# Kernel optimization log

Measured on AMD Instinct MI355X. Metric: run time of the kernel, lower is better.

Reference implementation:

```python
import jax, jax.numpy as jnp
import numpy as np

B, CIN, COUT, H, W, K = 32, 256, 256, 56, 56, 3
STRIDE, PAD, DIL = 1, 1, 1
SPARSITY = 0.9  # fraction of weight entries pruned to zero


def setup_inputs() -> dict:
    key = jax.random.key(0)
    kx, kw, km = jax.random.split(key, 3)
    x = jax.random.normal(kx, (B, CIN, H, W), dtype=jnp.float32)
    w = jax.random.normal(kw, (COUT, CIN, K, K), dtype=jnp.float32)
    mask = (jax.random.uniform(km, (COUT, CIN, K, K)) > SPARSITY).astype(jnp.float32)
    w = w * mask
    return {"x": x, "weight": w}


def reference(x, weight):
    # Faithful math of SparseConv2D.forward (sparse path == nn.Conv2d, bias=None):
    # NCHW input, OIHW weight, stride/pad/dilation as configured.
    out = jax.lax.conv_general_dilated(
        x, weight,
        window_strides=(STRIDE, STRIDE),
        padding=[(PAD, PAD), (PAD, PAD)],
        rhs_dilation=(DIL, DIL),
        dimension_numbers=("NCHW", "OIHW", "NCHW"),
    )
    return out  # [B, COUT, H_out, W_out]
```

## Files before the change

kernel.cpp:

```cpp
#include <hip/hip_runtime.h>
#include <hip/hip_bf16.h>


typedef __attribute__((ext_vector_type(8))) short short8;
typedef __attribute__((ext_vector_type(4))) float f32x4;
typedef __attribute__((ext_vector_type(4))) int i32x4;

constexpr int BB = 32, CIN = 256, COUT = 256, H = 56, W = 56, HW = H * W;
constexpr int HP = 58, WP = 58;
constexpr int XSTR = 40, WSTR = 40;

constexpr size_t XP_ELEMS = (size_t)BB * HP * WP * CIN;
constexpr size_t WB_ELEMS = (size_t)COUT * 9 * CIN;
constexpr size_t WS_NEEDED = (XP_ELEMS + WB_ELEMS) * 2;

__device__ __forceinline__ ushort f2bf(float f) {
    unsigned x = __float_as_uint(f);
    unsigned r = (x + 0x7FFFu + ((x >> 16) & 1u)) >> 16;
    return (ushort)r;
}


__global__ __launch_bounds__(256)
void prep_xp(const float* __restrict__ x, ushort* __restrict__ xp) {
    const int bi = blockIdx.x;
    const int b = bi / HP, i = bi % HP;
    ushort* dst = xp + (size_t)bi * WP * CIN;
    const int t = threadIdx.x;
    if (i == 0 || i == HP - 1) {
        for (int c = 0; c < WP; ++c) dst[c * CIN + t] = 0;
    } else {
        const float* src = x + ((size_t)b * CIN + t) * HW + (size_t)(i - 1) * W;
        dst[0 * CIN + t] = 0;
        dst[(WP - 1) * CIN + t] = 0;
        for (int c = 1; c <= W; ++c)
            dst[c * CIN + t] = f2bf(src[c - 1]);
    }
}

__global__ __launch_bounds__(256)
void prep_wb(const float* __restrict__ w, ushort* __restrict__ wb) {
    const int d = blockIdx.x * 256 + threadIdx.x;
    const int cin = d & 255;
    const int rest = d >> 8;
    const int tap = rest % 9;
    const int cout = rest / 9;
    wb[d] = f2bf(w[((size_t)cout * CIN + cin) * 9 + tap]);
}


__global__ __launch_bounds__(256)
void conv_mfma(const ushort* __restrict__ xp, const ushort* __restrict__ wb,
               float* __restrict__ out) {
    int bx = blockIdx.x;
    bx = (bx & 7) * 224 + (bx >> 3);

    const int mt = bx & 1;
    const int nt = bx >> 1;
    const int b  = nt / 28;
    const int h0 = (nt % 28) * 2;

    const int tid  = threadIdx.x;
    const int wv   = tid >> 6;
    const int lane = tid & 63;
    const int ml   = lane & 15;
    const int g    = lane >> 4;

    __shared__ ushort xs[4 * WP * XSTR];
    __shared__ ushort wt[128 * WSTR];

    const int aoff0 = (wv * 32 + ml) * WSTR + 8 * g;
    const int aoff1 = aoff0 + 16 * WSTR;
    int boff[7];
    #pragma unroll
    for (int nf = 0; nf < 7; ++nf) {
        const int p = nf * 16 + ml;
        const int hl = (p >= 56) ? 1 : 0;
        const int wl = p - 56 * hl;
        boff[nf] = (hl * WP + wl) * XSTR + 8 * g;
    }

    f32x4 acc[2][7] = {};

    const size_t xp_base = (size_t)(b * HP + h0) * WP * CIN;

    for (int cb = 0; cb < 8; ++cb) {
        __syncthreads();
        if (tid < 4 * WP) {
            const int r = tid / WP, c = tid % WP;
            const i32x4* src = (const i32x4*)(xp + xp_base + (size_t)(r * WP + c) * CIN + cb * 32);
            ushort* d = &xs[(r * WP + c) * XSTR];
            #pragma unroll
            for (int i = 0; i < 4; ++i) *(i32x4*)(d + i * 8) = src[i];
        }
        {
            const int cout = tid >> 1, half = tid & 1;
            const i32x4* src = (const i32x4*)(wb + (size_t)((mt * 128 + cout) * 9 + 0) * CIN
                                              + cb * 32 + half * 16);
            ushort* d = &wt[cout * WSTR + half * 16];
            i32x4 v0 = src[0], v1 = src[1];
            *(i32x4*)d = v0; *(i32x4*)(d + 8) = v1;
        }
        __syncthreads();

        for (int tap = 0; tap < 9; ++tap) {
            const int kh = tap / 3, kw = tap % 3;
            const int toff = (kh * WP + kw) * XSTR;

            const short8 a0 = *(const short8*)&wt[aoff0];
            const short8 a1 = *(const short8*)&wt[aoff1];
            #pragma unroll
            for (int nf = 0; nf < 7; ++nf) {
                const short8 bf = *(const short8*)&xs[boff[nf] + toff];
                acc[0][nf] = __builtin_amdgcn_mfma_f32_16x16x32_bf16(a0, bf, acc[0][nf], 0, 0, 0);
                acc[1][nf] = __builtin_amdgcn_mfma_f32_16x16x32_bf16(a1, bf, acc[1][nf], 0, 0, 0);
            }

            if (tap < 8) {
                __syncthreads();
                const int cout = tid >> 1, half = tid & 1;
                const i32x4* src = (const i32x4*)(wb + (size_t)((mt * 128 + cout) * 9 + tap + 1) * CIN
                                                  + cb * 32 + half * 16);
                ushort* d = &wt[cout * WSTR + half * 16];
                i32x4 v0 = src[0], v1 = src[1];
                *(i32x4*)d = v0; *(i32x4*)(d + 8) = v1;
                __syncthreads();
            }
        }
    }

    float* ob = out + ((size_t)b * COUT + mt * 128 + wv * 32) * HW;
    #pragma unroll
    for (int fm = 0; fm < 2; ++fm)
        #pragma unroll
        for (int nf = 0; nf < 7; ++nf)
            #pragma unroll
            for (int r = 0; r < 4; ++r) {
                const int cout_l = fm * 16 + 4 * g + r;
                const int p = nf * 16 + ml;
                const int hh = (p >= 56) ? 1 : 0;
                const int ww = p - 56 * hh;
                ob[(size_t)cout_l * HW + (h0 + hh) * W + ww] = acc[fm][nf][r];
            }
}


constexpr int WSZ = CIN * 9;
constexpr int NIN = 54 * 54;

__global__ __launch_bounds__(256)
void sparse_conv3x3(const float* __restrict__ x,
                    const float* __restrict__ wgt,
                    float* __restrict__ out) {
    const int bc = blockIdx.x, cout = bc % COUT, b = bc / COUT;
    const int tid = threadIdx.x;
    __shared__ int2 s_ent[WSZ];
    __shared__ unsigned char s_kk[WSZ];
    __shared__ int s_cnt[257];
    const float* wc = wgt + (size_t)cout * WSZ;
    float mv[9]; int cnt = 0;
    #pragma unroll
    for (int i = 0; i < 9; ++i) { mv[i] = wc[tid * 9 + i]; if (mv[i] != 0.0f) cnt++; }
    s_cnt[tid] = cnt; __syncthreads();
    if (tid == 0) { int run = 0; for (int t = 0; t < 256; ++t) { int c = s_cnt[t]; s_cnt[t] = run; run += c; } s_cnt[256] = run; }
    __syncthreads();
    { int pos = s_cnt[tid];
      #pragma unroll
      for (int i = 0; i < 9; ++i) if (mv[i] != 0.0f) {
          const int kh = i / 3, kw = i - kh * 3;
          int2 e; e.x = (tid * HW + (kh - 1) * W + (kw - 1)) * 4; e.y = __float_as_int(mv[i]);
          s_ent[pos] = e; s_kk[pos] = (unsigned char)(kh | (kw << 4)); pos++; } }
    __syncthreads();
    const int nnz = s_cnt[256];
    const char* xb = (const char*)(x + (size_t)b * CIN * HW);
    float* ob = out + (size_t)bc * HW;
    for (int o = tid; o < HW; o += 256) {
        int h, w; bool interior = (o < NIN);
        if (interior) { h = 1 + o / 54; w = 1 + (o - (h - 1) * 54); }
        else { int o2 = o - NIN;
            if (o2 < 56) { h = 0; w = o2; } else if (o2 < 112) { h = 55; w = o2 - 56; }
            else if (o2 < 166) { h = 1 + (o2 - 112); w = 0; } else { h = 1 + (o2 - 166); w = 55; } }
        const char* pb = xb + (size_t)(h * W + w) * 4;
        float acc = 0.0f;
        if (interior) {
            #pragma unroll 4
            for (int e = 0; e < nnz; ++e) { const int2 en = s_ent[e];
                acc = fmaf(__int_as_float(en.y), *(const float*)(pb + en.x), acc); }
        } else {
            const int h1 = h - 1, w1 = w - 1;
            for (int e = 0; e < nnz; ++e) { const int2 en = s_ent[e]; const int kk = s_kk[e];
                const int hh = h1 + (kk & 15), ww = w1 + (kk >> 4);
                if ((unsigned)hh < (unsigned)H && (unsigned)ww < (unsigned)W)
                    acc = fmaf(__int_as_float(en.y), *(const float*)(pb + en.x), acc); } }
        ob[h * W + w] = acc;
    }
}


extern "C" void kernel_launch(void* const* d_in, const int* in_sizes, int n_in,
                              void* d_out, int out_size, void* d_ws, size_t ws_size,
                              hipStream_t stream) {
    const float* x = (const float*)d_in[0];
    const float* w = (const float*)d_in[1];
    float* out = (float*)d_out;

    if (ws_size >= WS_NEEDED) {
        ushort* xp = (ushort*)d_ws;
        ushort* wbp = xp + XP_ELEMS;
        prep_xp<<<BB * HP, 256, 0, stream>>>(x, xp);
        prep_wb<<<(int)(WB_ELEMS / 256), 256, 0, stream>>>(w, wbp);
        conv_mfma<<<1792, 256, 0, stream>>>(xp, wbp, out);
    } else {
        sparse_conv3x3<<<BB * COUT, 256, 0, stream>>>(x, w, out);
    }
}
```

Before: 177.2 us.

## Load weights directly to registers, prefetch input tiles, transpose prep via LDS

The conv kernel no longer stages weights in shared memory. Each lane now reads its A fragments straight from global memory, with the next tap prefetched into registers, which removes two barriers per tap. Input channel-block tiles are register-prefetched one iteration ahead so the global loads overlap the MFMA work, and launch bounds now request two blocks per SM. The input prep kernel transposes through LDS so its global reads are coalesced. The cost is more global weight traffic per block, served from cache, and higher register pressure.

```diff
diff --git a/kernel.cpp b/kernel.cpp
--- a/kernel.cpp
+++ b/kernel.cpp
@@ -1,5 +1,4 @@
 #include <hip/hip_runtime.h>
-#include <hip/hip_bf16.h>
 
 
 typedef __attribute__((ext_vector_type(8))) short short8;
@@ -8,7 +7,7 @@
 
 constexpr int BB = 32, CIN = 256, COUT = 256, H = 56, W = 56, HW = H * W;
 constexpr int HP = 58, WP = 58;
-constexpr int XSTR = 40, WSTR = 40;
+constexpr int XSTR = 40;
 
 constexpr size_t XP_ELEMS = (size_t)BB * HP * WP * CIN;
 constexpr size_t WB_ELEMS = (size_t)COUT * 9 * CIN;
@@ -26,16 +25,24 @@
     const int bi = blockIdx.x;
     const int b = bi / HP, i = bi % HP;
     ushort* dst = xp + (size_t)bi * WP * CIN;
-    const int t = threadIdx.x;
+    const int tid = threadIdx.x;
+
     if (i == 0 || i == HP - 1) {
-        for (int c = 0; c < WP; ++c) dst[c * CIN + t] = 0;
-    } else {
-        const float* src = x + ((size_t)b * CIN + t) * HW + (size_t)(i - 1) * W;
-        dst[0 * CIN + t] = 0;
-        dst[(WP - 1) * CIN + t] = 0;
-        for (int c = 1; c <= W; ++c)
-            dst[c * CIN + t] = f2bf(src[c - 1]);
-    }
+        i32x4 z = {0, 0, 0, 0};
+        for (int k = tid; k < WP * CIN / 8; k += 256) ((i32x4*)dst)[k] = z;
+        return;
+    }
+
+    __shared__ ushort t[W][CIN + 2];
+    const int lane = tid & 63, wv = tid >> 6;
+    if (lane < W) {
+        const float* src = x + (size_t)b * CIN * HW + (size_t)(i - 1) * W + lane;
+        for (int cin = wv; cin < CIN; cin += 4)
+            t[lane][cin] = f2bf(src[(size_t)cin * HW]);
+    }
+    __syncthreads();
+    for (int c = 0; c < WP; ++c)
+        dst[c * CIN + tid] = (c == 0 || c == WP - 1) ? (ushort)0 : t[c - 1][tid];
 }
 
 __global__ __launch_bounds__(256)
@@ -49,7 +56,7 @@
 }
 
 
-__global__ __launch_bounds__(256)
+__global__ __launch_bounds__(256, 2)
 void conv_mfma(const ushort* __restrict__ xp, const ushort* __restrict__ wb,
                float* __restrict__ out) {
     int bx = blockIdx.x;
@@ -67,10 +74,10 @@
     const int g    = lane >> 4;
 
     __shared__ ushort xs[4 * WP * XSTR];
-    __shared__ ushort wt[128 * WSTR];
-
-    const int aoff0 = (wv * 32 + ml) * WSTR + 8 * g;
-    const int aoff1 = aoff0 + 16 * WSTR;
+
+    const ushort* wb0 = wb + (size_t)(mt * 128 + wv * 32 + ml) * 9 * CIN + 8 * g;
+    const ushort* wb1 = wb0 + (size_t)16 * 9 * CIN;
+
     int boff[7];
     #pragma unroll
     for (int nf = 0; nf < 7; ++nf) {
@@ -80,52 +87,53 @@
         boff[nf] = (hl * WP + wl) * XSTR + 8 * g;
     }
 
+    const int sr = tid / WP, sc = tid % WP;
+    const bool do_stage = (tid < 4 * WP);
+    const ushort* sp = xp + ((size_t)(b * HP + h0) * WP + sr * WP + sc) * CIN;
+    ushort* sd = &xs[(sr * WP + sc) * XSTR];
+
     f32x4 acc[2][7] = {};
-
-    const size_t xp_base = (size_t)(b * HP + h0) * WP * CIN;
+    i32x4 stg[4];
+
+    if (do_stage) {
+        const i32x4* s = (const i32x4*)sp;
+        stg[0] = s[0]; stg[1] = s[1]; stg[2] = s[2]; stg[3] = s[3];
+    }
 
     for (int cb = 0; cb < 8; ++cb) {
         __syncthreads();
-        if (tid < 4 * WP) {
-            const int r = tid / WP, c = tid % WP;
-            const i32x4* src = (const i32x4*)(xp + xp_base + (size_t)(r * WP + c) * CIN + cb * 32);
-            ushort* d = &xs[(r * WP + c) * XSTR];
-            #pragma unroll
-            for (int i = 0; i < 4; ++i) *(i32x4*)(d + i * 8) = src[i];
+        if (do_stage) {
+            *(i32x4*)(sd)      = stg[0];
+            *(i32x4*)(sd + 8)  = stg[1];
+            *(i32x4*)(sd + 16) = stg[2];
+            *(i32x4*)(sd + 24) = stg[3];
         }
-        {
-            const int cout = tid >> 1, half = tid & 1;
-            const i32x4* src = (const i32x4*)(wb + (size_t)((mt * 128 + cout) * 9 + 0) * CIN
-                                              + cb * 32 + half * 16);
-            ushort* d = &wt[cout * WSTR + half * 16];
-            i32x4 v0 = src[0], v1 = src[1];
-            *(i32x4*)d = v0; *(i32x4*)(d + 8) = v1;
+        if (cb < 7 && do_stage) {
+            const i32x4* s = (const i32x4*)(sp + (cb + 1) * 32);
+            stg[0] = s[0]; stg[1] = s[1]; stg[2] = s[2]; stg[3] = s[3];
         }
         __syncthreads();
 
+        const ushort* wa0 = wb0 + cb * 32;
+        const ushort* wa1 = wb1 + cb * 32;
+        short8 a0 = *(const short8*)wa0;
+        short8 a1 = *(const short8*)wa1;
+        #pragma unroll
         for (int tap = 0; tap < 9; ++tap) {
-            const int kh = tap / 3, kw = tap % 3;
+            short8 n0, n1;
+            if (tap < 8) {
+                n0 = *(const short8*)(wa0 + (tap + 1) * CIN);
+                n1 = *(const short8*)(wa1 + (tap + 1) * CIN);
+            }
+            const int kh = tap / 3, kw = tap - kh * 3;
             const int toff = (kh * WP + kw) * XSTR;
-
-            const short8 a0 = *(const short8*)&wt[aoff0];
-            const short8 a1 = *(const short8*)&wt[aoff1];
             #pragma unroll
             for (int nf = 0; nf < 7; ++nf) {
                 const short8 bf = *(const short8*)&xs[boff[nf] + toff];
                 acc[0][nf] = __builtin_amdgcn_mfma_f32_16x16x32_bf16(a0, bf, acc[0][nf], 0, 0, 0);
                 acc[1][nf] = __builtin_amdgcn_mfma_f32_16x16x32_bf16(a1, bf, acc[1][nf], 0, 0, 0);
             }
-
-            if (tap < 8) {
-                __syncthreads();
-                const int cout = tid >> 1, half = tid & 1;
-                const i32x4* src = (const i32x4*)(wb + (size_t)((mt * 128 + cout) * 9 + tap + 1) * CIN
-                                                  + cb * 32 + half * 16);
-                ushort* d = &wt[cout * WSTR + half * 16];
-                i32x4 v0 = src[0], v1 = src[1];
-                *(i32x4*)d = v0; *(i32x4*)(d + 8) = v1;
-                __syncthreads();
-            }
+            if (tap < 8) { a0 = n0; a1 = n1; }
         }
     }
 
```

Result: slower. 188.7 us (+6.5%).
